# Optimization experiments

Hardware: AMD Instinct MI355X
Metric: run time of the kernel (lower is better)

## Reference

```python
import jax, jax.numpy as jnp
import numpy as np
from jax import lax

B, T, K = 1024, 512, 32


def setup_inputs() -> dict:
    key = jax.random.key(0)
    k1, k2, k3 = jax.random.split(key, 3)
    labels = jax.random.randint(k1, (B, T), 0, K, dtype=jnp.int32)
    y_pred = jax.random.normal(k2, (B, T, K), dtype=jnp.float32)
    # glorot-uniform-ish transition matrix
    limit = np.sqrt(6.0 / (K + K)).astype(np.float32)
    trans = jax.random.uniform(k3, (K, K), minval=-limit, maxval=limit, dtype=jnp.float32)
    mask = jnp.ones((B, T), dtype=jnp.float32)
    return {"labels": labels, "y_pred": y_pred, "trans": trans, "mask": mask}


def crf_loss(labels, y_pred, trans, mask):
    n_tags = trans.shape[0]
    y_true = jax.nn.one_hot(labels, n_tags, dtype=y_pred.dtype)  # [B,T,K]
    y_true = y_true * mask[:, :, None]  # sequence_masking with value 0

    # --- target path score ---
    point_score = jnp.einsum('bni,bni->b', y_true, y_pred)
    trans_score = jnp.einsum('bni,ij,bnj->b', y_true[:, :-1], trans, y_true[:, 1:])
    target = point_score + trans_score

    # --- log partition via forward algorithm (logsumexp scan) ---
    alpha0 = y_pred[:, 0]  # [B,K]

    def step(alpha, xs):
        emit, m = xs  # emit: [B,K], m: [B,1]
        new = jax.nn.logsumexp(alpha[:, :, None] + trans[None], axis=1) + emit
        alpha = m * new + (1.0 - m) * alpha
        return alpha, None

    xs = (jnp.swapaxes(y_pred[:, 1:], 0, 1),          # [T-1,B,K]
          jnp.swapaxes(mask[:, 1:, None], 0, 1))      # [T-1,B,1]
    alpha, _ = lax.scan(step, alpha0, xs)
    log_norm = jax.nn.logsumexp(alpha, axis=1)  # [B]
    return log_norm - target


def reference(labels, y_pred, trans, mask):
    return crf_loss(labels, y_pred, trans, mask)
```

## Files before the change

kernel.cpp:

```cpp
#include <hip/hip_runtime.h>


#define K32 32
#define Tt  512
#define NCH 8
#define CHL 64
#define NST 2
#define STL 32

typedef float  float4v __attribute__((ext_vector_type(4)));
typedef short  short8v __attribute__((ext_vector_type(8)));

__device__ inline float bf2f_lo(unsigned d) { return __uint_as_float(d << 16); }
__device__ inline float bf2f_hi(unsigned d) { return __uint_as_float(d & 0xFFFF0000u); }

__device__ inline unsigned pack_trunc(float hi, float lo) {
    return __builtin_amdgcn_perm(__float_as_uint(hi), __float_as_uint(lo), 0x07060302u);
}
__device__ inline unsigned short f2bf_rne(float x) {
    unsigned u = __float_as_uint(x);
    return (unsigned short)((u + 0x7FFFu + ((u >> 16) & 1u)) >> 16);
}

union F8 { unsigned u[4]; short8v v; };

__global__ __launch_bounds__(512, 8) void crf_fused(
    const int*   __restrict__ labels,
    const float* __restrict__ y_pred,
    const float* __restrict__ trans,
    const float* __restrict__ mask,
    float*       __restrict__ out)
{
    __shared__ float expAll[8][1024];

    const int lane = threadIdx.x & 63;
    const int wv   = __builtin_amdgcn_readfirstlane(threadIdx.x >> 6);
    const int n    = lane & 15;
    const int q    = lane >> 4;
    const int seq  = blockIdx.x;
    const int c    = wv;

    float* eb = &expAll[wv][0];

    const float* yp  = y_pred + (size_t)seq * Tt * K32;
    const int*   lb  = labels + (size_t)seq * Tt;
    const float* mkp = mask   + (size_t)seq * Tt;
    const int tbase = c * CHL;

    float4 pre[4];
    {
        const float4* gs = (const float4*)(yp + (size_t)tbase * K32);
#pragma unroll
        for (int jj = 0; jj < 4; ++jj) pre[jj] = gs[jj * 64 + lane];
    }

    float sc;
    float mlane;
    {
        const int t = tbase + lane;
        const int lab0 = lb[t];
        mlane = mkp[t];
        sc = yp[t * K32 + lab0] * mlane;
        if (t < Tt - 1) {
            sc += trans[lab0 * K32 + lb[t + 1]] * (mlane * mkp[t + 1]);
        }
#pragma unroll
        for (int s = 1; s < 64; s <<= 1) sc += __shfl_xor(sc, s, 64);
    }
    unsigned long long mbits = __ballot(mlane != 0.0f);
    if (c == 0) mbits &= ~1ull;
    const int applied = __popcll(mbits);

    F8 AE0, AE1;
#pragma unroll
    for (int h = 0; h < 4; ++h) {
        const int k0 = (h < 2) ? (q * 4 + 2 * h) : (16 + q * 4 + 2 * (h - 2));
        const int k1 = k0 + 1;
        AE0.u[h] = ((unsigned)f2bf_rne(__expf(trans[k0 * K32 + n]) * 0.03125f)) |
                   (((unsigned)f2bf_rne(__expf(trans[k1 * K32 + n]) * 0.03125f)) << 16);
        AE1.u[h] = ((unsigned)f2bf_rne(__expf(trans[k0 * K32 + 16 + n]) * 0.03125f)) |
                   (((unsigned)f2bf_rne(__expf(trans[k1 * K32 + 16 + n]) * 0.03125f)) << 16);
    }

    F8 B0, B1;
#pragma unroll
    for (int h = 0; h < 4; ++h) {
        const int r0 = (h < 2) ? (q * 4 + 2 * h) : (16 + q * 4 + 2 * (h - 2));
        const int r1 = r0 + 1;
        unsigned w0 = 0, w1 = 0;
        if (r0 == n)      w0 |= 0x3F80u;
        if (r1 == n)      w0 |= 0x3F800000u;
        if (r0 == 16 + n) w1 |= 0x3F80u;
        if (r1 == 16 + n) w1 |= 0x3F800000u;
        B0.u[h] = w0;
        B1.u[h] = w1;
    }

    const float4v zf = {0.f, 0.f, 0.f, 0.f};
    float Slog = 0.0f;

    const int svoff0 = q * 4;
    const int svoff1 = 16 + q * 4;

    auto step = [&](int i, bool ren) {
        const float4v sv0 = *(const float4v*)&eb[i * 32 + svoff0];
        const float4v sv1 = *(const float4v*)&eb[i * 32 + svoff1];

        float4v c00 = __builtin_amdgcn_mfma_f32_16x16x32_bf16(AE0.v, B0.v, zf, 0, 0, 0);
        float4v c01 = __builtin_amdgcn_mfma_f32_16x16x32_bf16(AE0.v, B1.v, zf, 0, 0, 0);
        float4v c10 = __builtin_amdgcn_mfma_f32_16x16x32_bf16(AE1.v, B0.v, zf, 0, 0, 0);
        float4v c11 = __builtin_amdgcn_mfma_f32_16x16x32_bf16(AE1.v, B1.v, zf, 0, 0, 0);

        c00 *= sv0; c01 *= sv0; c10 *= sv1; c11 *= sv1;

        if (ren) {
            const float cn = __uint_as_float(
                __builtin_amdgcn_readfirstlane(__float_as_uint(c00[0])));
            const float rs = 1.0f / cn;
            c00 *= rs; c01 *= rs; c10 *= rs; c11 *= rs;
            Slog += __logf(cn);
        }

        B0.u[0] = pack_trunc(c00[1], c00[0]);
        B0.u[1] = pack_trunc(c00[3], c00[2]);
        B0.u[2] = pack_trunc(c10[1], c10[0]);
        B0.u[3] = pack_trunc(c10[3], c10[2]);
        B1.u[0] = pack_trunc(c01[1], c01[0]);
        B1.u[1] = pack_trunc(c01[3], c01[2]);
        B1.u[2] = pack_trunc(c11[1], c11[0]);
        B1.u[3] = pack_trunc(c11[3], c11[2]);
    };

    for (int st = 0; st < NST; ++st) {
#pragma unroll
        for (int jj = 0; jj < 4; ++jj) {
            const float4 pv = pre[jj];
            float4v e;
            e[0] = __expf(pv.x); e[1] = __expf(pv.y);
            e[2] = __expf(pv.z); e[3] = __expf(pv.w);
            *(float4v*)&eb[(jj * 64 + lane) * 4] = e;
        }
        if (st + 1 < NST) {
            const float4* gs = (const float4*)(yp + (size_t)(tbase + (st + 1) * STL) * K32);
#pragma unroll
            for (int jj = 0; jj < 4; ++jj) pre[jj] = gs[jj * 64 + lane];
        }

        const unsigned b32 = (unsigned)(mbits >> (st * 32));
        if (b32 == 0xFFFFFFFFu) {
#pragma unroll
            for (int g = 0; g < 4; ++g) {
                step(g * 8 + 0, false); step(g * 8 + 1, false);
                step(g * 8 + 2, false); step(g * 8 + 3, false);
                step(g * 8 + 4, false); step(g * 8 + 5, false);
                step(g * 8 + 6, false); step(g * 8 + 7, true);
            }
        } else if (b32 == 0xFFFFFFFEu) {
#pragma unroll
            for (int g = 0; g < 4; ++g) {
                if (g != 0) step(g * 8 + 0, false);
                step(g * 8 + 1, false); step(g * 8 + 2, false);
                step(g * 8 + 3, false); step(g * 8 + 4, false);
                step(g * 8 + 5, false); step(g * 8 + 6, false);
                step(g * 8 + 7, true);
            }
        } else {
            for (int i = 0; i < STL; ++i) {
                if ((b32 >> i) & 1u) step(i, (i & 7) == 7);
            }
        }
    }

    {
        unsigned* Nd = (unsigned*)eb;
        *(uint2*)&Nd[n * 20 + q * 2]            = make_uint2(B0.u[0], B0.u[1]);
        *(uint2*)&Nd[n * 20 + 8 + q * 2]        = make_uint2(B0.u[2], B0.u[3]);
        *(uint2*)&Nd[(16 + n) * 20 + q * 2]     = make_uint2(B1.u[0], B1.u[1]);
        *(uint2*)&Nd[(16 + n) * 20 + 8 + q * 2] = make_uint2(B1.u[2], B1.u[3]);
    }
    {
        const unsigned short* Ncm = (const unsigned short*)eb;
        unsigned r[8];
#pragma unroll
        for (int ii = 0; ii < 8; ++ii) {
            const int idx = ii * 64 + lane;
            const int k = idx >> 4, d = idx & 15;
            r[ii] = (unsigned)Ncm[(2 * d) * 40 + k] |
                    ((unsigned)Ncm[(2 * d + 1) * 40 + k] << 16);
        }
        unsigned* md = (unsigned*)eb;
#pragma unroll
        for (int ii = 0; ii < 8; ++ii) md[ii * 64 + lane] = r[ii];
    }
    if (lane == 0) {
        eb[1016] = Slog + (float)applied * 3.46573590f;
        eb[1017] = sc;
    }

    __syncthreads();

    if (wv == 0) {
        const int h = lane >> 5;
        const int j = lane & 31;

        uint4 cA, cB;
        {
            const unsigned* mt = (const unsigned*)&expAll[0][0];
            cA = *(const uint4*)&mt[j * 16 + 8 * h];
            cB = *(const uint4*)&mt[j * 16 + 8 * h + 4];
        }

        const float a0 = yp[j];
        const float m0 = __shfl(a0, 0, 64);
        float p = __expf(a0 - m0);
        float S = m0;

        float scs = 0.0f;
#pragma unroll
        for (int cc = 0; cc < NCH; ++cc) {
            S   += expAll[cc][1016];
            scs += expAll[cc][1017];
        }

        const int cb = h << 4;
#pragma unroll
        for (int cc = 0; cc < NCH; ++cc) {
            uint4 nA = {0, 0, 0, 0}, nB = {0, 0, 0, 0};
            if (cc + 1 < NCH) {
                const unsigned* mt = (const unsigned*)&expAll[cc + 1][0];
                nA = *(const uint4*)&mt[j * 16 + 8 * h];
                nB = *(const uint4*)&mt[j * 16 + 8 * h + 4];
            }
            const float cn = __shfl(p, 0, 64);
            const unsigned u0 = cA.x, u1 = cA.y, u2 = cA.z, u3 = cA.w;
            const unsigned u4 = cB.x, u5 = cB.y, u6 = cB.z, u7 = cB.w;
            float acc = 0.0f;
            acc = fmaf(__shfl(p, cb +  0, 64), bf2f_lo(u0), acc);
            acc = fmaf(__shfl(p, cb +  1, 64), bf2f_hi(u0), acc);
            acc = fmaf(__shfl(p, cb +  2, 64), bf2f_lo(u1), acc);
            acc = fmaf(__shfl(p, cb +  3, 64), bf2f_hi(u1), acc);
            acc = fmaf(__shfl(p, cb +  4, 64), bf2f_lo(u2), acc);
            acc = fmaf(__shfl(p, cb +  5, 64), bf2f_hi(u2), acc);
            acc = fmaf(__shfl(p, cb +  6, 64), bf2f_lo(u3), acc);
            acc = fmaf(__shfl(p, cb +  7, 64), bf2f_hi(u3), acc);
            acc = fmaf(__shfl(p, cb +  8, 64), bf2f_lo(u4), acc);
            acc = fmaf(__shfl(p, cb +  9, 64), bf2f_hi(u4), acc);
            acc = fmaf(__shfl(p, cb + 10, 64), bf2f_lo(u5), acc);
            acc = fmaf(__shfl(p, cb + 11, 64), bf2f_hi(u5), acc);
            acc = fmaf(__shfl(p, cb + 12, 64), bf2f_lo(u6), acc);
            acc = fmaf(__shfl(p, cb + 13, 64), bf2f_hi(u6), acc);
            acc = fmaf(__shfl(p, cb + 14, 64), bf2f_lo(u7), acc);
            acc = fmaf(__shfl(p, cb + 15, 64), bf2f_hi(u7), acc);
            acc += __shfl_xor(acc, 32, 64);
            p = acc * (1.0f / cn);
            S += __logf(cn);
            cA = nA; cB = nB;
        }

        float sp = p;
        sp += __shfl_xor(sp,  1, 64);
        sp += __shfl_xor(sp,  2, 64);
        sp += __shfl_xor(sp,  4, 64);
        sp += __shfl_xor(sp,  8, 64);
        sp += __shfl_xor(sp, 16, 64);

        if (lane == 0) {
            out[seq] = S + __logf(sp) - scs;
        }
    }
}

extern "C" void kernel_launch(void* const* d_in, const int* in_sizes, int n_in,
                              void* d_out, int out_size, void* d_ws, size_t ws_size,
                              hipStream_t stream) {
    const int*   labels = (const int*)  d_in[0];
    const float* y_pred = (const float*)d_in[1];
    const float* trans  = (const float*)d_in[2];
    const float* mask   = (const float*)d_in[3];
    float* out = (float*)d_out;

    crf_fused<<<1024, 512, 0, stream>>>(labels, y_pred, trans, mask, out);
}
```

Measured before the change: 148.9 us.

## Interleave two chunk chains per wave and use exponent-only renormalization

Each block now uses 4 waves instead of 8, and each wave advances two independent 64-step chunk recurrences in alternation, so the MFMA latency of one chain can be hidden behind the other. Renormalization now takes the power of two from the float exponent bits instead of computing a reciprocal and a log. The y_pred prefetch for the second half is no longer overlapped; it is loaded right before use. This gives more instruction-level parallelism per wave at the cost of fewer waves per block and more registers.

After: 135.4 us. 9.0% less time.

```diff
diff --git a/kernel.cpp b/kernel.cpp
--- a/kernel.cpp
+++ b/kernel.cpp
@@ -24,52 +24,62 @@
 
 union F8 { unsigned u[4]; short8v v; };
 
-__global__ __launch_bounds__(512, 8) void crf_fused(
+__global__ __launch_bounds__(256, 4) void crf_fused(
     const int*   __restrict__ labels,
     const float* __restrict__ y_pred,
     const float* __restrict__ trans,
     const float* __restrict__ mask,
     float*       __restrict__ out)
 {
-    __shared__ float expAll[8][1024];
+    __shared__ float expAll[4][2048];
+    __shared__ float sAux[8];
 
     const int lane = threadIdx.x & 63;
     const int wv   = __builtin_amdgcn_readfirstlane(threadIdx.x >> 6);
     const int n    = lane & 15;
     const int q    = lane >> 4;
     const int seq  = blockIdx.x;
-    const int c    = wv;
-
-    float* eb = &expAll[wv][0];
+
+    float* ebA = &expAll[wv][0];
+    float* ebB = ebA + 1024;
 
     const float* yp  = y_pred + (size_t)seq * Tt * K32;
     const int*   lb  = labels + (size_t)seq * Tt;
     const float* mkp = mask   + (size_t)seq * Tt;
-    const int tbase = c * CHL;
-
-    float4 pre[4];
+    const int tbA = wv * 128;
+    const int tbB = tbA + 64;
+
+    float4 preA[4], preB[4];
     {
-        const float4* gs = (const float4*)(yp + (size_t)tbase * K32);
-#pragma unroll
-        for (int jj = 0; jj < 4; ++jj) pre[jj] = gs[jj * 64 + lane];
+        const float4* gA = (const float4*)(yp + (size_t)tbA * K32);
+        const float4* gB = (const float4*)(yp + (size_t)tbB * K32);
+#pragma unroll
+        for (int jj = 0; jj < 4; ++jj) { preA[jj] = gA[jj * 64 + lane]; preB[jj] = gB[jj * 64 + lane]; }
     }
 
     float sc;
-    float mlane;
+    float mA, mB;
     {
-        const int t = tbase + lane;
-        const int lab0 = lb[t];
-        mlane = mkp[t];
-        sc = yp[t * K32 + lab0] * mlane;
-        if (t < Tt - 1) {
-            sc += trans[lab0 * K32 + lb[t + 1]] * (mlane * mkp[t + 1]);
-        }
-#pragma unroll
-        for (int s = 1; s < 64; s <<= 1) sc += __shfl_xor(sc, s, 64);
-    }
-    unsigned long long mbits = __ballot(mlane != 0.0f);
-    if (c == 0) mbits &= ~1ull;
-    const int applied = __popcll(mbits);
+        const int tA = tbA + lane;
+        const int labA = lb[tA];
+        mA = mkp[tA];
+        float s = yp[tA * K32 + labA] * mA;
+        s += trans[labA * K32 + lb[tA + 1]] * (mA * mkp[tA + 1]);
+
+        const int tB = tbB + lane;
+        const int labB = lb[tB];
+        mB = mkp[tB];
+        float sB = yp[tB * K32 + labB] * mB;
+        if (tB < Tt - 1) sB += trans[labB * K32 + lb[tB + 1]] * (mB * mkp[tB + 1]);
+
+        sc = s + sB;
+#pragma unroll
+        for (int sft = 1; sft < 64; sft <<= 1) sc += __shfl_xor(sc, sft, 64);
+    }
+    unsigned long long mbA = __ballot(mA != 0.0f);
+    unsigned long long mbB = __ballot(mB != 0.0f);
+    if (wv == 0) mbA &= ~1ull;
+    const int applied = __popcll(mbA) + __popcll(mbB);
 
     F8 AE0, AE1;
 #pragma unroll
@@ -82,7 +92,7 @@
                    (((unsigned)f2bf_rne(__expf(trans[k1 * K32 + 16 + n]) * 0.03125f)) << 16);
     }
 
-    F8 B0, B1;
+    F8 BA0, BA1, BB0, BB1;
 #pragma unroll
     for (int h = 0; h < 4; ++h) {
         const int r0 = (h < 2) ? (q * 4 + 2 * h) : (16 + q * 4 + 2 * (h - 2));
@@ -92,19 +102,19 @@
         if (r1 == n)      w0 |= 0x3F800000u;
         if (r0 == 16 + n) w1 |= 0x3F80u;
         if (r1 == 16 + n) w1 |= 0x3F800000u;
-        B0.u[h] = w0;
-        B1.u[h] = w1;
+        BA0.u[h] = w0; BA1.u[h] = w1;
+        BB0.u[h] = w0; BB1.u[h] = w1;
     }
 
     const float4v zf = {0.f, 0.f, 0.f, 0.f};
-    float Slog = 0.0f;
+    int eSum = 0;
 
     const int svoff0 = q * 4;
     const int svoff1 = 16 + q * 4;
 
-    auto step = [&](int i, bool ren) {
-        const float4v sv0 = *(const float4v*)&eb[i * 32 + svoff0];
-        const float4v sv1 = *(const float4v*)&eb[i * 32 + svoff1];
+    auto stepone = [&](const float* ebx, F8& B0, F8& B1, int i, bool ren) {
+        const float4v sv0 = *(const float4v*)&ebx[i * 32 + svoff0];
+        const float4v sv1 = *(const float4v*)&ebx[i * 32 + svoff1];
 
         float4v c00 = __builtin_amdgcn_mfma_f32_16x16x32_bf16(AE0.v, B0.v, zf, 0, 0, 0);
         float4v c01 = __builtin_amdgcn_mfma_f32_16x16x32_bf16(AE0.v, B1.v, zf, 0, 0, 0);
@@ -114,11 +124,11 @@
         c00 *= sv0; c01 *= sv0; c10 *= sv1; c11 *= sv1;
 
         if (ren) {
-            const float cn = __uint_as_float(
-                __builtin_amdgcn_readfirstlane(__float_as_uint(c00[0])));
-            const float rs = 1.0f / cn;
+            const unsigned cb = __builtin_amdgcn_readfirstlane(__float_as_uint(c00[0]));
+            const int e = (int)((cb >> 23) & 255u) - 127;
+            const float rs = __uint_as_float((unsigned)(127 - e) << 23);
             c00 *= rs; c01 *= rs; c10 *= rs; c11 *= rs;
-            Slog += __logf(cn);
+            eSum += e;
         }
 
         B0.u[0] = pack_trunc(c00[1], c00[0]);
@@ -132,69 +142,109 @@
     };
 
     for (int st = 0; st < NST; ++st) {
-#pragma unroll
-        for (int jj = 0; jj < 4; ++jj) {
-            const float4 pv = pre[jj];
-            float4v e;
-            e[0] = __expf(pv.x); e[1] = __expf(pv.y);
-            e[2] = __expf(pv.z); e[3] = __expf(pv.w);
-            *(float4v*)&eb[(jj * 64 + lane) * 4] = e;
-        }
-        if (st + 1 < NST) {
-            const float4* gs = (const float4*)(yp + (size_t)(tbase + (st + 1) * STL) * K32);
-#pragma unroll
-            for (int jj = 0; jj < 4; ++jj) pre[jj] = gs[jj * 64 + lane];
-        }
-
-        const unsigned b32 = (unsigned)(mbits >> (st * 32));
-        if (b32 == 0xFFFFFFFFu) {
-#pragma unroll
+        if (st == 0) {
+#pragma unroll
+            for (int jj = 0; jj < 4; ++jj) {
+                float4v eA, eB;
+                eA[0] = __expf(preA[jj].x); eA[1] = __expf(preA[jj].y);
+                eA[2] = __expf(preA[jj].z); eA[3] = __expf(preA[jj].w);
+                eB[0] = __expf(preB[jj].x); eB[1] = __expf(preB[jj].y);
+                eB[2] = __expf(preB[jj].z); eB[3] = __expf(preB[jj].w);
+                *(float4v*)&ebA[(jj * 64 + lane) * 4] = eA;
+                *(float4v*)&ebB[(jj * 64 + lane) * 4] = eB;
+            }
+        } else {
+            const float4* gA = (const float4*)(yp + (size_t)(tbA + STL) * K32);
+            const float4* gB = (const float4*)(yp + (size_t)(tbB + STL) * K32);
+#pragma unroll
+            for (int jj = 0; jj < 4; ++jj) {
+                const float4 pA = gA[jj * 64 + lane];
+                const float4 pB = gB[jj * 64 + lane];
+                float4v eA, eB;
+                eA[0] = __expf(pA.x); eA[1] = __expf(pA.y);
+                eA[2] = __expf(pA.z); eA[3] = __expf(pA.w);
+                eB[0] = __expf(pB.x); eB[1] = __expf(pB.y);
+                eB[2] = __expf(pB.z); eB[3] = __expf(pB.w);
+                *(float4v*)&ebA[(jj * 64 + lane) * 4] = eA;
+                *(float4v*)&ebB[(jj * 64 + lane) * 4] = eB;
+            }
+        }
+
+        const unsigned bA = (unsigned)(mbA >> (st * 32));
+        const unsigned bB = (unsigned)(mbB >> (st * 32));
+        if (bA == 0xFFFFFFFFu && bB == 0xFFFFFFFFu) {
             for (int g = 0; g < 4; ++g) {
-                step(g * 8 + 0, false); step(g * 8 + 1, false);
-                step(g * 8 + 2, false); step(g * 8 + 3, false);
-                step(g * 8 + 4, false); step(g * 8 + 5, false);
-                step(g * 8 + 6, false); step(g * 8 + 7, true);
-            }
-        } else if (b32 == 0xFFFFFFFEu) {
-#pragma unroll
+                const int i0 = g * 8;
+                stepone(ebA, BA0, BA1, i0 + 0, false); stepone(ebB, BB0, BB1, i0 + 0, false);
+                stepone(ebA, BA0, BA1, i0 + 1, false); stepone(ebB, BB0, BB1, i0 + 1, false);
+                stepone(ebA, BA0, BA1, i0 + 2, false); stepone(ebB, BB0, BB1, i0 + 2, false);
+                stepone(ebA, BA0, BA1, i0 + 3, false); stepone(ebB, BB0, BB1, i0 + 3, false);
+                stepone(ebA, BA0, BA1, i0 + 4, false); stepone(ebB, BB0, BB1, i0 + 4, false);
+                stepone(ebA, BA0, BA1, i0 + 5, false); stepone(ebB, BB0, BB1, i0 + 5, false);
+                stepone(ebA, BA0, BA1, i0 + 6, false); stepone(ebB, BB0, BB1, i0 + 6, false);
+                stepone(ebA, BA0, BA1, i0 + 7, true);  stepone(ebB, BB0, BB1, i0 + 7, true);
+            }
+        } else if (bA == 0xFFFFFFFEu && bB == 0xFFFFFFFFu) {
             for (int g = 0; g < 4; ++g) {
-                if (g != 0) step(g * 8 + 0, false);
-                step(g * 8 + 1, false); step(g * 8 + 2, false);
-                step(g * 8 + 3, false); step(g * 8 + 4, false);
-                step(g * 8 + 5, false); step(g * 8 + 6, false);
-                step(g * 8 + 7, true);
+                const int i0 = g * 8;
+                if (g != 0) stepone(ebA, BA0, BA1, i0 + 0, false);
+                stepone(ebB, BB0, BB1, i0 + 0, false);
+                stepone(ebA, BA0, BA1, i0 + 1, false); stepone(ebB, BB0, BB1, i0 + 1, false);
+                stepone(ebA, BA0, BA1, i0 + 2, false); stepone(ebB, BB0, BB1, i0 + 2, false);
+                stepone(ebA, BA0, BA1, i0 + 3, false); stepone(ebB, BB0, BB1, i0 + 3, false);
+                stepone(ebA, BA0, BA1, i0 + 4, false); stepone(ebB, BB0, BB1, i0 + 4, false);
+                stepone(ebA, BA0, BA1, i0 + 5, false); stepone(ebB, BB0, BB1, i0 + 5, false);
+                stepone(ebA, BA0, BA1, i0 + 6, false); stepone(ebB, BB0, BB1, i0 + 6, false);
+                stepone(ebA, BA0, BA1, i0 + 7, true);  stepone(ebB, BB0, BB1, i0 + 7, true);
             }
         } else {
             for (int i = 0; i < STL; ++i) {
-                if ((b32 >> i) & 1u) step(i, (i & 7) == 7);
+                const bool ren = (i & 7) == 7;
+                if ((bA >> i) & 1u) stepone(ebA, BA0, BA1, i, ren);
+                if ((bB >> i) & 1u) stepone(ebB, BB0, BB1, i, ren);
             }
         }
     }
 
     {
-        unsigned* Nd = (unsigned*)eb;
-        *(uint2*)&Nd[n * 20 + q * 2]            = make_uint2(B0.u[0], B0.u[1]);
-        *(uint2*)&Nd[n * 20 + 8 + q * 2]        = make_uint2(B0.u[2], B0.u[3]);
-        *(uint2*)&Nd[(16 + n) * 20 + q * 2]     = make_uint2(B1.u[0], B1.u[1]);
-        *(uint2*)&Nd[(16 + n) * 20 + 8 + q * 2] = make_uint2(B1.u[2], B1.u[3]);
-    }
-    {
-        const unsigned short* Ncm = (const unsigned short*)eb;
-        unsigned r[8];
+        unsigned* scr = (unsigned*)ebA + 1024;
+        unsigned* md  = (unsigned*)ebA;
+
+        *(uint2*)&scr[n * 20 + q * 2]            = make_uint2(BA0.u[0], BA0.u[1]);
+        *(uint2*)&scr[n * 20 + 8 + q * 2]        = make_uint2(BA0.u[2], BA0.u[3]);
+        *(uint2*)&scr[(16 + n) * 20 + q * 2]     = make_uint2(BA1.u[0], BA1.u[1]);
+        *(uint2*)&scr[(16 + n) * 20 + 8 + q * 2] = make_uint2(BA1.u[2], BA1.u[3]);
+        const unsigned short* NcA = (const unsigned short*)scr;
+        unsigned rA[8];
 #pragma unroll
         for (int ii = 0; ii < 8; ++ii) {
             const int idx = ii * 64 + lane;
             const int k = idx >> 4, d = idx & 15;
-            r[ii] = (unsigned)Ncm[(2 * d) * 40 + k] |
-                    ((unsigned)Ncm[(2 * d + 1) * 40 + k] << 16);
-        }
-        unsigned* md = (unsigned*)eb;
-#pragma unroll
-        for (int ii = 0; ii < 8; ++ii) md[ii * 64 + lane] = r[ii];
+            rA[ii] = (unsigned)NcA[(2 * d) * 40 + k] |
+                     ((unsigned)NcA[(2 * d + 1) * 40 + k] << 16);
+        }
+#pragma unroll
+        for (int ii = 0; ii < 8; ++ii) md[ii * 64 + lane] = rA[ii];
+
+        *(uint2*)&scr[n * 20 + q * 2]            = make_uint2(BB0.u[0], BB0.u[1]);
+        *(uint2*)&scr[n * 20 + 8 + q * 2]        = make_uint2(BB0.u[2], BB0.u[3]);
+        *(uint2*)&scr[(16 + n) * 20 + q * 2]     = make_uint2(BB1.u[0], BB1.u[1]);
+        *(uint2*)&scr[(16 + n) * 20 + 8 + q * 2] = make_uint2(BB1.u[2], BB1.u[3]);
+        const unsigned short* NcB = (const unsigned short*)scr;
+        unsigned rB[8];
+#pragma unroll
+        for (int ii = 0; ii < 8; ++ii) {
+            const int idx = ii * 64 + lane;
+            const int k = idx >> 4, d = idx & 15;
+            rB[ii] = (unsigned)NcB[(2 * d) * 40 + k] |
+                     ((unsigned)NcB[(2 * d + 1) * 40 + k] << 16);
+        }
+#pragma unroll
+        for (int ii = 0; ii < 8; ++ii) md[512 + ii * 64 + lane] = rB[ii];
     }
     if (lane == 0) {
-        eb[1016] = Slog + (float)applied * 3.46573590f;
-        eb[1017] = sc;
+        sAux[wv]     = (float)eSum * 0.693147180559945f + (float)applied * 3.46573590f;
+        sAux[4 + wv] = sc;
     }
 
     __syncthreads();
@@ -203,12 +253,12 @@
         const int h = lane >> 5;
         const int j = lane & 31;
 
-        uint4 cA, cB;
-        {
-            const unsigned* mt = (const unsigned*)&expAll[0][0];
-            cA = *(const uint4*)&mt[j * 16 + 8 * h];
-            cB = *(const uint4*)&mt[j * 16 + 8 * h + 4];
-        }
+        auto mt = [&](int cc) -> const unsigned* {
+            return (const unsigned*)&expAll[cc >> 1][0] + ((cc & 1) << 9);
+        };
+
+        uint4 cA = *(const uint4*)&mt(0)[j * 16 + 8 * h];
+        uint4 cB = *(const uint4*)&mt(0)[j * 16 + 8 * h + 4];
 
         const float a0 = yp[j];
         const float m0 = __shfl(a0, 0, 64);
@@ -217,19 +267,15 @@
 
         float scs = 0.0f;
 #pragma unroll
-        for (int cc = 0; cc < NCH; ++cc) {
-            S   += expAll[cc][1016];
-            scs += expAll[cc][1017];
-        }
+        for (int w = 0; w < 4; ++w) { S += sAux[w]; scs += sAux[4 + w]; }
 
         const int cb = h << 4;
 #pragma unroll
         for (int cc = 0; cc < NCH; ++cc) {
             uint4 nA = {0, 0, 0, 0}, nB = {0, 0, 0, 0};
             if (cc + 1 < NCH) {
-                const unsigned* mt = (const unsigned*)&expAll[cc + 1][0];
-                nA = *(const uint4*)&mt[j * 16 + 8 * h];
-                nB = *(const uint4*)&mt[j * 16 + 8 * h + 4];
+                nA = *(const uint4*)&mt(cc + 1)[j * 16 + 8 * h];
+                nB = *(const uint4*)&mt(cc + 1)[j * 16 + 8 * h + 4];
             }
             const float cn = __shfl(p, 0, 64);
             const unsigned u0 = cA.x, u1 = cA.y, u2 = cA.z, u3 = cA.w;
@@ -279,5 +325,5 @@
     const float* mask   = (const float*)d_in[3];
     float* out = (float*)d_out;
 
-    crf_fused<<<1024, 512, 0, stream>>>(labels, y_pred, trans, mask, out);
+    crf_fused<<<1024, 256, 0, stream>>>(labels, y_pred, trans, mask, out);
 }
```
